# Performance work log

Hardware: AMD Instinct MI355X
Metric: run time of the kernel (lower is better)

## Reference

```python
import math
import jax, jax.numpy as jnp
import numpy as np


def conv2d(x, w, b, pad=0, dil=1):
    # x: [B, Cin, H, W], w: [Cout, Cin, kh, kw] (OIHW)
    y = jax.lax.conv_general_dilated(
        x, w, window_strides=(1, 1),
        padding=[(pad, pad), (pad, pad)],
        rhs_dilation=(dil, dil),
        dimension_numbers=('NCHW', 'OIHW', 'NCHW'))
    return y + b[None, :, None, None]


def setup_inputs() -> dict:
    key = jax.random.key(0)
    ks = jax.random.split(key, 8)
    B, C, H, W = 2, 64, 96, 96
    inner = 64 // 18  # = 3, as in the torch module
    n_dil = 3
    s = 0.1
    x = jax.random.normal(ks[0], (B, C, H, W), jnp.float32)
    w_red = jax.random.normal(ks[1], (inner, C, 1, 1), jnp.float32) * s
    b_red = jax.random.normal(ks[2], (inner,), jnp.float32) * s
    w_dil = jax.random.normal(ks[3], (n_dil, inner, inner, 3, 3), jnp.float32) * s
    b_dil = jax.random.normal(ks[4], (n_dil, inner), jnp.float32) * s
    w_fuse = jax.random.normal(ks[5], (C, inner * n_dil * 6, 1, 1), jnp.float32) * s
    b_fuse = jax.random.normal(ks[6], (C,), jnp.float32) * s
    return {"x": x, "w_red": w_red, "b_red": b_red, "w_dil": w_dil,
            "b_dil": b_dil, "w_fuse": w_fuse, "b_fuse": b_fuse}


def _c4_transforms(x):
    # identity, flip-W, flip-H, rot90 k=1,2,3 over spatial dims
    return [x,
            jnp.flip(x, axis=-1),
            jnp.flip(x, axis=-2),
            jnp.rot90(x, 1, axes=(2, 3)),
            jnp.rot90(x, 2, axes=(2, 3)),
            jnp.rot90(x, 3, axes=(2, 3))]


def reference(x, w_red, b_red, w_dil, b_dil, w_fuse, b_fuse):
    dilations = (1, 2, 3)
    residual_scale = 0.2
    B, C, H, W = x.shape
    x_red = conv2d(x, w_red, b_red)                    # [B, inner, H, W]
    tfs = _c4_transforms(x_red)
    feats = []
    for i, d in enumerate(dilations):
        co = conv2d(x_red, w_dil[i], b_dil[i], pad=d, dil=d)
        for tf in tfs:
            feats.append(co * tf)
    cat = jnp.concatenate(feats, axis=1)               # [B, inner*18, H, W]
    fused = conv2d(cat, w_fuse, b_fuse)                # [B, C, H, W]
    tokens = fused.reshape(B, C, H * W).transpose(0, 2, 1)  # [B, N, C]
    # Chunked attention in the original is mathematically full self-attention
    scores = jnp.einsum('bnc,bmc->bnm', tokens, tokens) / math.sqrt(C)
    attn = jax.nn.softmax(scores, axis=-1)
    out = jnp.einsum('bnm,bmc->bnc', attn, tokens)     # [B, N, C]
    out = out.transpose(0, 2, 1).reshape(B, C, H, W)
    return x + residual_scale * out
```

## Files before the change

### kernel.cpp

```cpp
#include <hip/hip_runtime.h>

#define HW    96
#define NPIX  9216
#define NCH   64
#define INNER 3
#define NDIL  3
#define BB    2
#define TOTPIX (BB * NPIX)
#define NT32  (NPIX / 32)

typedef __attribute__((ext_vector_type(8))) short short8;
typedef __attribute__((ext_vector_type(8))) unsigned short ushort8;
typedef __attribute__((ext_vector_type(4))) float f32x4;
typedef __attribute__((ext_vector_type(4))) unsigned int uint32x4;

__device__ __forceinline__ ushort f2bf_rne(float f) {
    unsigned u = __float_as_uint(f);
    u += 0x7fffu + ((u >> 16) & 1u);
    return (ushort)(u >> 16);
}
__device__ __forceinline__ float bf2f(ushort u) {
    return __uint_as_float((unsigned)u << 16);
}
__device__ __forceinline__ unsigned pack_bf(float lo, float hi) {
    return __builtin_amdgcn_perm(__float_as_uint(hi), __float_as_uint(lo), 0x07060302u);
}

__global__ __launch_bounds__(256) void
k_reduce(const float* __restrict__ x, const float* __restrict__ w_red,
         const float* __restrict__ b_red, float* __restrict__ xred,
         float* __restrict__ L) {
    __shared__ float part[4][3][64];
    int tid = threadIdx.x;
    int gid = blockIdx.x * 256 + tid;
    if (gid < TOTPIX) L[gid] = 0.f;
    int cp = tid >> 6, lane = tid & 63;
    int pix = blockIdx.x * 64 + lane;
    int b = pix / NPIX, n = pix % NPIX;
    const float* xb = x + (size_t)b * NCH * NPIX + (size_t)(cp * 16) * NPIX + n;
    float a0 = 0.f, a1 = 0.f, a2 = 0.f;
    #pragma unroll
    for (int c = 0; c < 16; ++c) {
        float xv = xb[(size_t)c * NPIX];
        a0 = fmaf(w_red[0 * NCH + cp * 16 + c], xv, a0);
        a1 = fmaf(w_red[1 * NCH + cp * 16 + c], xv, a1);
        a2 = fmaf(w_red[2 * NCH + cp * 16 + c], xv, a2);
    }
    part[cp][0][lane] = a0; part[cp][1][lane] = a1; part[cp][2][lane] = a2;
    __syncthreads();
    if (tid < 192) {
        int o = tid >> 6, lp = tid & 63;
        float s = ((part[0][o][lp] + part[1][o][lp]) +
                   (part[2][o][lp] + part[3][o][lp])) + b_red[o];
        int pix2 = blockIdx.x * 64 + lp;
        int b2 = pix2 / NPIX, n2 = pix2 % NPIX;
        xred[((size_t)b2 * INNER + o) * NPIX + n2] = s;
    }
}

__global__ __launch_bounds__(256) void
k_feat(const float* __restrict__ xred, const float* __restrict__ w_dil,
       const float* __restrict__ b_dil, ushort* __restrict__ FT) {
    int gid = blockIdx.x * 256 + threadIdx.x;
    int io = gid / TOTPIX;
    int pix = gid - io * TOTPIX;
    int i3 = io / 3, o = io - 3 * i3;
    int b = pix / NPIX, n = pix % NPIX;
    int h = n / HW, w = n % HW;
    const float* xr = xred + (size_t)b * INNER * NPIX;
    int d = i3 + 1;

    float co = b_dil[i3 * 3 + o];
    #pragma unroll
    for (int ci = 0; ci < 3; ++ci) {
        const float* xo = xr + ci * NPIX;
        #pragma unroll
        for (int kh = 0; kh < 3; ++kh) {
            int hh = h + (kh - 1) * d;
            #pragma unroll
            for (int kw = 0; kw < 3; ++kw) {
                int ww = w + (kw - 1) * d;
                float v = ((unsigned)hh < HW && (unsigned)ww < HW) ? xo[hh * HW + ww] : 0.f;
                co = fmaf(w_dil[(9 * i3 + 3 * o + ci) * 9 + kh * 3 + kw], v, co);
            }
        }
    }

    const float* xo = xr + o * NPIX;
    float tf0 = xo[h * HW + w];
    float tf1 = xo[h * HW + (HW - 1 - w)];
    float tf2 = xo[(HW - 1 - h) * HW + w];
    float tf3 = xo[w * HW + (HW - 1 - h)];
    float tf4 = xo[(HW - 1 - h) * HW + (HW - 1 - w)];
    float tf5 = xo[(HW - 1 - w) * HW + h];

    size_t base = (size_t)(i3 * 18 + o) * TOTPIX + pix;
    FT[base + (size_t)(0 * 3) * TOTPIX] = f2bf_rne(co * tf0);
    FT[base + (size_t)(1 * 3) * TOTPIX] = f2bf_rne(co * tf1);
    FT[base + (size_t)(2 * 3) * TOTPIX] = f2bf_rne(co * tf2);
    FT[base + (size_t)(3 * 3) * TOTPIX] = f2bf_rne(co * tf3);
    FT[base + (size_t)(4 * 3) * TOTPIX] = f2bf_rne(co * tf4);
    FT[base + (size_t)(5 * 3) * TOTPIX] = f2bf_rne(co * tf5);
}

__global__ __launch_bounds__(256) void
k_fuse(const ushort* __restrict__ FT, const float* __restrict__ w_fuse,
       const float* __restrict__ b_fuse, ushort* __restrict__ tok,
       ushort* __restrict__ tokTt) {
    __shared__ ushort wpad[64 * 72];
    __shared__ float  bsh[64];
    __shared__ ushort tile[64 * 72];

    int tid = threadIdx.x;
    for (int i = tid; i < 64 * 64; i += 256) {
        int c = i >> 6, j = i & 63;
        wpad[c * 72 + j] = (j < 54) ? f2bf_rne(w_fuse[c * 54 + j]) : (ushort)0;
    }
    if (tid < 64) bsh[tid] = b_fuse[tid];
    __syncthreads();

    int wv = tid >> 6, lane = tid & 63, quad = lane >> 4, l15 = lane & 15;
    int px0 = blockIdx.x * 64;

    short8 af[4][2];
    #pragma unroll
    for (int m = 0; m < 4; ++m)
        #pragma unroll
        for (int kc = 0; kc < 2; ++kc)
            af[m][kc] = *(const short8*)&wpad[(16 * m + l15) * 72 + quad * 8 + 32 * kc];

    f32x4 acc[4];
    #pragma unroll
    for (int m = 0; m < 4; ++m) acc[m] = (f32x4){0.f, 0.f, 0.f, 0.f};

    int px = px0 + wv * 16 + l15;
    #pragma unroll
    for (int kc = 0; kc < 2; ++kc) {
        short8 bf;
        #pragma unroll
        for (int jj = 0; jj < 8; ++jj)
            bf[jj] = (short)FT[(size_t)(quad * 8 + jj + 32 * kc) * TOTPIX + px];
        #pragma unroll
        for (int m = 0; m < 4; ++m)
            acc[m] = __builtin_amdgcn_mfma_f32_16x16x32_bf16(af[m][kc], bf, acc[m], 0, 0, 0);
    }

    #pragma unroll
    for (int m = 0; m < 4; ++m)
        #pragma unroll
        for (int r = 0; r < 4; ++r) {
            int c = 16 * m + quad * 4 + r;
            tile[c * 72 + wv * 16 + l15] = f2bf_rne(acc[m][r] + bsh[c]);
        }
    __syncthreads();

    int b0 = px0 / NPIX, n0 = px0 % NPIX;
    {
        int lp = tid >> 2, part = tid & 3;
        ushort row[16];
        #pragma unroll
        for (int k = 0; k < 16; ++k) row[k] = tile[(part * 16 + k) * 72 + lp];
        ushort* dst = tok + ((size_t)b0 * NPIX + n0 + lp) * NCH + part * 16;
        *(ushort8*)&dst[0] = *(const ushort8*)&row[0];
        *(ushort8*)&dst[8] = *(const ushort8*)&row[8];
    }
    {
        int c = tid >> 2, seg = tid & 3;
        int n = n0 + seg * 16;
        size_t base = (((size_t)b0 * NT32 + (n >> 5)) * 64 + c) * 32 + (n & 31);
        *(ushort8*)&tokTt[base]     = *(const ushort8*)&tile[c * 72 + seg * 16];
        *(ushort8*)&tokTt[base + 8] = *(const ushort8*)&tile[c * 72 + seg * 16 + 8];
    }
}

__global__ __launch_bounds__(256, 5) void
k_attn(const ushort* __restrict__ tok, const ushort* __restrict__ tokTt,
       float* __restrict__ L, ushort* __restrict__ pacc, int P, int KP) {
    __shared__ ushort smem[9728];
    ushort* ldsK = smem;
    ushort* ldsV = smem + 4608;

    const int QW = NPIX / 128;
    int bid0 = blockIdx.x;
    int nwg = gridDim.x;
    int bid = (bid0 & 7) * (nwg >> 3) + (bid0 >> 3);
    int qc = bid % QW; int rest = bid / QW;
    int p = rest % P;  int b = rest / P;
    int tid = threadIdx.x;
    int wv = tid >> 6, lane = tid & 63;
    int quad = lane >> 4, l15 = lane & 15;

    const ushort* tb  = tok + (size_t)b * NPIX * NCH;
    const ushort* tvb = tokTt + (size_t)b * NT32 * (64 * 32);
    int qwave = qc * 128 + wv * 32;

    int sk_off = (tid >> 3) * 72 + (tid & 7) * 8;
    int svj = tid & 3;
    int sv_b0 = (tid >> 2) * 40 + 8 * ((2 * svj) & 3) + 4 * (svj >> 1);
    int sv_b1 = (tid >> 2) * 40 + 8 * ((2 * svj + 1) & 3) + 4 * (svj >> 1);

    short8 qf[2][2];
    const float scale = 0.125f * 1.44269504088896340736f;
    #pragma unroll
    for (int n = 0; n < 2; ++n) {
        const ushort* qr = tb + (size_t)(qwave + 16 * n + l15) * NCH + quad * 8;
        #pragma unroll
        for (int kc = 0; kc < 2; ++kc) {
            ushort8 raw = *(const ushort8*)(qr + 32 * kc);
            short8 f;
            #pragma unroll
            for (int e = 0; e < 8; ++e) f[e] = (short)f2bf_rne(bf2f(raw[e]) * scale);
            qf[n][kc] = f;
        }
    }

    f32x4 O[4][2];
    #pragma unroll
    for (int m = 0; m < 4; ++m)
        #pragma unroll
        for (int n = 0; n < 2; ++n) O[m][n] = (f32x4){0.f, 0.f, 0.f, 0.f};
    float lrun[2] = {0.f, 0.f};

    const float FM = 16.0f;
    const f32x4 FMc = (f32x4){-FM, -FM, -FM, -FM};

    int k0 = p * KP;
    int nt = KP / 32;

    const ushort* pK = tb + (size_t)k0 * NCH + tid * 8;
    const ushort* pV = tvb + ((size_t)(k0 >> 5)) * 2048 + tid * 8;

    {
        ushort8 gK = *(const ushort8*)pK;
        ushort8 gV = *(const ushort8*)pV;
        *(ushort8*)&ldsK[sk_off] = gK;
        uint32x4 v4 = *(uint32x4*)&gV;
        *(uint2*)&ldsV[sv_b0] = make_uint2(v4.x, v4.y);
        *(uint2*)&ldsV[sv_b1] = make_uint2(v4.z, v4.w);
    }
    __syncthreads();

    for (int t = 0; t < nt; ++t) {
        int curK = (t & 1) * 2304, curV = (t & 1) * 2560;
        bool pre = (t + 1 < nt);
        pK += 32 * NCH;  pV += 2048;

        ushort8 nK, nV;
        if (pre) {
            nK = *(const ushort8*)pK;
            nV = *(const ushort8*)pV;
        }

        short8 kd[4];
        #pragma unroll
        for (int m2 = 0; m2 < 2; ++m2)
            #pragma unroll
            for (int kc = 0; kc < 2; ++kc)
                kd[2 * m2 + kc] = *(const short8*)&ldsK[curK + (16 * m2 + l15) * 72 +
                                                       quad * 8 + 32 * kc];

        uint32x4 wac[2];
        #pragma unroll
        for (int m2 = 0; m2 < 2; ++m2) {
            f32x4 Sm[2];
            __builtin_amdgcn_s_setprio(1);
            #pragma unroll
            for (int n = 0; n < 2; ++n) {
                Sm[n] = __builtin_amdgcn_mfma_f32_16x16x32_bf16(kd[2 * m2 + 0],
                                                                qf[n][0], FMc, 0, 0, 0);
                Sm[n] = __builtin_amdgcn_mfma_f32_16x16x32_bf16(kd[2 * m2 + 1],
                                                                qf[n][1], Sm[n], 0, 0, 0);
            }
            __builtin_amdgcn_s_setprio(0);
            #pragma unroll
            for (int n = 0; n < 2; ++n) {
                float e0 = __builtin_amdgcn_exp2f(Sm[n][0]);
                float e1 = __builtin_amdgcn_exp2f(Sm[n][1]);
                float e2 = __builtin_amdgcn_exp2f(Sm[n][2]);
                float e3 = __builtin_amdgcn_exp2f(Sm[n][3]);
                lrun[n] += (e0 + e1) + (e2 + e3);
                if (m2 == 0) {
                    wac[n].x = pack_bf(e0, e1); wac[n].y = pack_bf(e2, e3);
                } else {
                    wac[n].z = pack_bf(e0, e1); wac[n].w = pack_bf(e2, e3);
                }
            }
        }

        if (pre) {
            *(ushort8*)&ldsK[(curK ^ 2304) + sk_off] = nK;
            uint32x4 v4 = *(uint32x4*)&nV;
            *(uint2*)&ldsV[(curV ^ 2560) + sv_b0] = make_uint2(v4.x, v4.y);
            *(uint2*)&ldsV[(curV ^ 2560) + sv_b1] = make_uint2(v4.z, v4.w);
        }

        short8 vf[4];
        #pragma unroll
        for (int mc = 0; mc < 4; ++mc)
            vf[mc] = *(const short8*)&ldsV[curV + (16 * mc + l15) * 40 + quad * 8];

        __builtin_amdgcn_s_setprio(1);
        #pragma unroll
        for (int n = 0; n < 2; ++n) {
            short8 bfr = *(short8*)&wac[n];
            #pragma unroll
            for (int mc = 0; mc < 4; ++mc)
                O[mc][n] = __builtin_amdgcn_mfma_f32_16x16x32_bf16(vf[mc], bfr,
                                                                   O[mc][n], 0, 0, 0);
        }
        __builtin_amdgcn_s_setprio(0);

        __syncthreads();
    }

    #pragma unroll
    for (int n = 0; n < 2; ++n) {
        lrun[n] += __shfl_xor(lrun[n], 16, 64);
        lrun[n] += __shfl_xor(lrun[n], 32, 64);
    }
    if (quad == 0) {
        #pragma unroll
        for (int n = 0; n < 2; ++n)
            atomicAdd(&L[(size_t)b * NPIX + qwave + 16 * n + l15], lrun[n]);
    }

    #pragma unroll
    for (int n = 0; n < 2; ++n) {
        int ql = wv * 32 + 16 * n + l15;
        #pragma unroll
        for (int m = 0; m < 4; ++m)
            #pragma unroll
            for (int r = 0; r < 4; ++r)
                smem[(16 * m + quad * 4 + r) * 136 + ql] = f2bf_rne(O[m][n][r]);
    }
    __syncthreads();
    size_t bp = (size_t)b * P + p;
    #pragma unroll
    for (int i = 0; i < 4; ++i) {
        int lin = i * 2048 + tid * 8;
        int c = lin >> 7, q = lin & 127;
        *(ushort8*)(pacc + (bp * NCH + c) * NPIX + qc * 128 + q) =
            *(const ushort8*)&smem[c * 136 + q];
    }
}

__global__ void k_combine(const float* __restrict__ x, const float* __restrict__ L,
                          const ushort* __restrict__ pacc, float* __restrict__ out,
                          int P) {
    int gid = blockIdx.x * blockDim.x + threadIdx.x;
    if (gid >= BB * NCH * (NPIX / 8)) return;
    int seg = gid % (NPIX / 8);
    int bc  = gid / (NPIX / 8);
    int b = bc / NCH;
    int n0 = seg * 8;
    float o[8] = {0.f, 0.f, 0.f, 0.f, 0.f, 0.f, 0.f, 0.f};
    for (int p = 0; p < P; ++p) {
        ushort8 t = *(const ushort8*)(pacc +
            (((size_t)b * P + p) * NCH + (bc % NCH)) * NPIX + n0);
        #pragma unroll
        for (int e = 0; e < 8; ++e) o[e] += bf2f(t[e]);
    }
    const float* lv = L + (size_t)b * NPIX + n0;
    const float* xb = x + (size_t)bc * NPIX + n0;
    float* ob = out + (size_t)bc * NPIX + n0;
    #pragma unroll
    for (int e = 0; e < 8; ++e)
        ob[e] = fmaf(0.2f / lv[e], o[e], xb[e]);
}

extern "C" void kernel_launch(void* const* d_in, const int* in_sizes, int n_in,
                              void* d_out, int out_size, void* d_ws, size_t ws_size,
                              hipStream_t stream) {
    const float* x      = (const float*)d_in[0];
    const float* w_red  = (const float*)d_in[1];
    const float* b_red  = (const float*)d_in[2];
    const float* w_dil  = (const float*)d_in[3];
    const float* b_dil  = (const float*)d_in[4];
    const float* w_fuse = (const float*)d_in[5];
    const float* b_fuse = (const float*)d_in[6];
    float* out = (float*)d_out;

    const size_t XRED_N = (size_t)BB * INNER * NPIX;
    const size_t FT_N   = (size_t)64 * TOTPIX;
    const size_t TOK_N  = (size_t)BB * NPIX * NCH;
    const size_t HEAD_B = XRED_N * 4 + (FT_N + 2 * TOK_N) * 2 + TOTPIX * 4;
    int P = 0;
    const int cands[4] = {8, 4, 2, 1};
    for (int ci = 0; ci < 4; ++ci) {
        int cp = cands[ci];
        size_t need = HEAD_B + (size_t)BB * cp * NPIX * NCH * 2;
        if (ws_size >= need) { P = cp; break; }
    }
    if (P == 0) return;

    float*  xred  = (float*)d_ws;
    ushort* FT    = (ushort*)(xred + XRED_N);
    ushort* tok   = FT + FT_N;
    ushort* tokTt = tok + TOK_N;
    float*  L     = (float*)(tokTt + TOK_N);
    ushort* pacc  = (ushort*)(L + TOTPIX);

    k_reduce <<<TOTPIX / 64, 256, 0, stream>>>(x, w_red, b_red, xred, L);
    k_feat   <<<9 * TOTPIX / 256, 256, 0, stream>>>(xred, w_dil, b_dil, FT);
    k_fuse   <<<TOTPIX / 64, 256, 0, stream>>>(FT, w_fuse, b_fuse, tok, tokTt);
    k_attn   <<<BB * P * (NPIX / 128), 256, 0, stream>>>(tok, tokTt, L, pacc,
                                                         P, NPIX / P);
    k_combine<<<(BB * NCH * (NPIX / 8) + 255) / 256, 256, 0, stream>>>(x, L, pacc,
                                                                       out, P);
}
```

Before: 137.2 us.

## Fuse dilated-conv feature generation into the fuse GEMM kernel via shared memory

Merges k_feat into k_fuse. Each block now computes its 64 pixels' 54 bf16 feature channels directly into an LDS tile instead of writing a global FT buffer and reading it back. This removes one kernel launch and the global round trip of FT (about 2.4 MB written and read). Each thread now handles all three output channels per dilation, reusing the loaded neighbors. In exchange, only 192 of 256 threads do the feature work, and the block adds an LDS tile plus a barrier.

```diff
diff --git a/kernel.cpp b/kernel.cpp
--- a/kernel.cpp
+++ b/kernel.cpp
@@ -59,56 +59,13 @@
 }
 
 __global__ __launch_bounds__(256) void
-k_feat(const float* __restrict__ xred, const float* __restrict__ w_dil,
-       const float* __restrict__ b_dil, ushort* __restrict__ FT) {
-    int gid = blockIdx.x * 256 + threadIdx.x;
-    int io = gid / TOTPIX;
-    int pix = gid - io * TOTPIX;
-    int i3 = io / 3, o = io - 3 * i3;
-    int b = pix / NPIX, n = pix % NPIX;
-    int h = n / HW, w = n % HW;
-    const float* xr = xred + (size_t)b * INNER * NPIX;
-    int d = i3 + 1;
-
-    float co = b_dil[i3 * 3 + o];
-    #pragma unroll
-    for (int ci = 0; ci < 3; ++ci) {
-        const float* xo = xr + ci * NPIX;
-        #pragma unroll
-        for (int kh = 0; kh < 3; ++kh) {
-            int hh = h + (kh - 1) * d;
-            #pragma unroll
-            for (int kw = 0; kw < 3; ++kw) {
-                int ww = w + (kw - 1) * d;
-                float v = ((unsigned)hh < HW && (unsigned)ww < HW) ? xo[hh * HW + ww] : 0.f;
-                co = fmaf(w_dil[(9 * i3 + 3 * o + ci) * 9 + kh * 3 + kw], v, co);
-            }
-        }
-    }
-
-    const float* xo = xr + o * NPIX;
-    float tf0 = xo[h * HW + w];
-    float tf1 = xo[h * HW + (HW - 1 - w)];
-    float tf2 = xo[(HW - 1 - h) * HW + w];
-    float tf3 = xo[w * HW + (HW - 1 - h)];
-    float tf4 = xo[(HW - 1 - h) * HW + (HW - 1 - w)];
-    float tf5 = xo[(HW - 1 - w) * HW + h];
-
-    size_t base = (size_t)(i3 * 18 + o) * TOTPIX + pix;
-    FT[base + (size_t)(0 * 3) * TOTPIX] = f2bf_rne(co * tf0);
-    FT[base + (size_t)(1 * 3) * TOTPIX] = f2bf_rne(co * tf1);
-    FT[base + (size_t)(2 * 3) * TOTPIX] = f2bf_rne(co * tf2);
-    FT[base + (size_t)(3 * 3) * TOTPIX] = f2bf_rne(co * tf3);
-    FT[base + (size_t)(4 * 3) * TOTPIX] = f2bf_rne(co * tf4);
-    FT[base + (size_t)(5 * 3) * TOTPIX] = f2bf_rne(co * tf5);
-}
-
-__global__ __launch_bounds__(256) void
-k_fuse(const ushort* __restrict__ FT, const float* __restrict__ w_fuse,
-       const float* __restrict__ b_fuse, ushort* __restrict__ tok,
-       ushort* __restrict__ tokTt) {
+k_featfuse(const float* __restrict__ xred, const float* __restrict__ w_dil,
+           const float* __restrict__ b_dil, const float* __restrict__ w_fuse,
+           const float* __restrict__ b_fuse, ushort* __restrict__ tok,
+           ushort* __restrict__ tokTt) {
     __shared__ ushort wpad[64 * 72];
     __shared__ float  bsh[64];
+    __shared__ ushort FTt[64 * 70];
     __shared__ ushort tile[64 * 72];
 
     int tid = threadIdx.x;
@@ -117,10 +74,61 @@
         wpad[c * 72 + j] = (j < 54) ? f2bf_rne(w_fuse[c * 54 + j]) : (ushort)0;
     }
     if (tid < 64) bsh[tid] = b_fuse[tid];
+
+    int px0 = blockIdx.x * 64;
+
+    if (tid < 192) {
+        int lp = tid & 63, i3 = tid >> 6;
+        int pix = px0 + lp;
+        int b = pix / NPIX, n = pix % NPIX;
+        int h = n / HW, w = n % HW;
+        const float* xr = xred + (size_t)b * INNER * NPIX;
+        int d = i3 + 1;
+
+        float co[3] = {b_dil[i3 * 3 + 0], b_dil[i3 * 3 + 1], b_dil[i3 * 3 + 2]};
+        #pragma unroll
+        for (int ci = 0; ci < 3; ++ci) {
+            const float* xo = xr + ci * NPIX;
+            #pragma unroll
+            for (int kh = 0; kh < 3; ++kh) {
+                int hh = h + (kh - 1) * d;
+                #pragma unroll
+                for (int kw = 0; kw < 3; ++kw) {
+                    int ww = w + (kw - 1) * d;
+                    float v = ((unsigned)hh < HW && (unsigned)ww < HW)
+                                  ? xo[hh * HW + ww] : 0.f;
+                    #pragma unroll
+                    for (int o = 0; o < 3; ++o)
+                        co[o] = fmaf(w_dil[(9 * i3 + 3 * o + ci) * 9 + kh * 3 + kw],
+                                     v, co[o]);
+                }
+            }
+        }
+
+        float tf[6][3];
+        #pragma unroll
+        for (int o = 0; o < 3; ++o) {
+            const float* xo = xr + o * NPIX;
+            tf[0][o] = xo[h * HW + w];
+            tf[1][o] = xo[h * HW + (HW - 1 - w)];
+            tf[2][o] = xo[(HW - 1 - h) * HW + w];
+            tf[3][o] = xo[w * HW + (HW - 1 - h)];
+            tf[4][o] = xo[(HW - 1 - h) * HW + (HW - 1 - w)];
+            tf[5][o] = xo[(HW - 1 - w) * HW + h];
+        }
+
+        #pragma unroll
+        for (int t = 0; t < 6; ++t)
+            #pragma unroll
+            for (int o = 0; o < 3; ++o)
+                FTt[(i3 * 18 + t * 3 + o) * 70 + lp] = f2bf_rne(co[o] * tf[t][o]);
+    } else {
+        for (int i = tid - 192; i < 640; i += 64)
+            FTt[(54 + (i >> 6)) * 70 + (i & 63)] = (ushort)0;
+    }
     __syncthreads();
 
     int wv = tid >> 6, lane = tid & 63, quad = lane >> 4, l15 = lane & 15;
-    int px0 = blockIdx.x * 64;
 
     short8 af[4][2];
     #pragma unroll
@@ -133,13 +141,13 @@
     #pragma unroll
     for (int m = 0; m < 4; ++m) acc[m] = (f32x4){0.f, 0.f, 0.f, 0.f};
 
-    int px = px0 + wv * 16 + l15;
+    int pxl = wv * 16 + l15;
     #pragma unroll
     for (int kc = 0; kc < 2; ++kc) {
         short8 bf;
         #pragma unroll
         for (int jj = 0; jj < 8; ++jj)
-            bf[jj] = (short)FT[(size_t)(quad * 8 + jj + 32 * kc) * TOTPIX + px];
+            bf[jj] = (short)FTt[(quad * 8 + jj + 32 * kc) * 70 + pxl];
         #pragma unroll
         for (int m = 0; m < 4; ++m)
             acc[m] = __builtin_amdgcn_mfma_f32_16x16x32_bf16(af[m][kc], bf, acc[m], 0, 0, 0);
@@ -381,9 +389,8 @@
     float* out = (float*)d_out;
 
     const size_t XRED_N = (size_t)BB * INNER * NPIX;
-    const size_t FT_N   = (size_t)64 * TOTPIX;
     const size_t TOK_N  = (size_t)BB * NPIX * NCH;
-    const size_t HEAD_B = XRED_N * 4 + (FT_N + 2 * TOK_N) * 2 + TOTPIX * 4;
+    const size_t HEAD_B = XRED_N * 4 + 2 * TOK_N * 2 + TOTPIX * 4;
     int P = 0;
     const int cands[4] = {8, 4, 2, 1};
     for (int ci = 0; ci < 4; ++ci) {
@@ -394,17 +401,16 @@
     if (P == 0) return;
 
     float*  xred  = (float*)d_ws;
-    ushort* FT    = (ushort*)(xred + XRED_N);
-    ushort* tok   = FT + FT_N;
+    ushort* tok   = (ushort*)(xred + XRED_N);
     ushort* tokTt = tok + TOK_N;
     float*  L     = (float*)(tokTt + TOK_N);
     ushort* pacc  = (ushort*)(L + TOTPIX);
 
-    k_reduce <<<TOTPIX / 64, 256, 0, stream>>>(x, w_red, b_red, xred, L);
-    k_feat   <<<9 * TOTPIX / 256, 256, 0, stream>>>(xred, w_dil, b_dil, FT);
-    k_fuse   <<<TOTPIX / 64, 256, 0, stream>>>(FT, w_fuse, b_fuse, tok, tokTt);
-    k_attn   <<<BB * P * (NPIX / 128), 256, 0, stream>>>(tok, tokTt, L, pacc,
-                                                         P, NPIX / P);
-    k_combine<<<(BB * NCH * (NPIX / 8) + 255) / 256, 256, 0, stream>>>(x, L, pacc,
-                                                                       out, P);
-}
+    k_reduce  <<<TOTPIX / 64, 256, 0, stream>>>(x, w_red, b_red, xred, L);
+    k_featfuse<<<TOTPIX / 64, 256, 0, stream>>>(xred, w_dil, b_dil, w_fuse,
+                                                b_fuse, tok, tokTt);
+    k_attn    <<<BB * P * (NPIX / 128), 256, 0, stream>>>(tok, tokTt, L, pacc,
+                                                          P, NPIX / P);
+    k_combine <<<(BB * NCH * (NPIX / 8) + 255) / 256, 256, 0, stream>>>(x, L, pacc,
+                                                                        out, P);
+}
```

Measured after the change: 137.8 us (median of 3 runs). No clear change (+0.4%).
